# Kernel optimization log

Measured on AMD Instinct MI355X. Metric: run time of the kernel, lower is better.

The kernel has to match this reference:

```python
import jax, jax.numpy as jnp
import numpy as np

N0, N1, N2 = 30000, 90000, 60000          # nodes, edges, triangles
D_IN, D_OUT, HEADS = 256, 128, 4
NNZ0, NNZ1, NNZ2 = 960000, 180000, 180000  # sparse incidence nnz


def setup_inputs() -> dict:
    key = jax.random.key(0)
    ks = jax.random.split(key, 18)
    s = 0.05
    return {
        "x0": jax.random.normal(ks[0], (N0, D_IN), dtype=jnp.float32),
        "x1": jax.random.normal(ks[1], (N1, D_IN), dtype=jnp.float32),
        "x2": jax.random.normal(ks[2], (N2, D_IN), dtype=jnp.float32),
        "rows0": jax.random.randint(ks[3], (NNZ0,), 0, N0),
        "cols0": jax.random.randint(ks[4], (NNZ0,), 0, N0),
        "rows1": jax.random.randint(ks[5], (NNZ1,), 0, N0),
        "cols1": jax.random.randint(ks[6], (NNZ1,), 0, N1),
        "rows2": jax.random.randint(ks[7], (NNZ2,), 0, N0),
        "cols2": jax.random.randint(ks[8], (NNZ2,), 0, N2),
        # per-head parameters (SATLayer_regular), stacked on leading head axis
        "W1": jax.random.normal(ks[9], (HEADS, D_IN, D_OUT), dtype=jnp.float32) * s,
        "b1": jax.random.normal(ks[10], (HEADS, D_OUT), dtype=jnp.float32) * s,
        "a1_w": jax.random.normal(ks[11], (HEADS, D_OUT), dtype=jnp.float32) * s,
        "a1_b": jax.random.normal(ks[12], (HEADS,), dtype=jnp.float32) * s,
        "a2_w": jax.random.normal(ks[13], (HEADS, D_OUT), dtype=jnp.float32) * s,
        "a2_b": jax.random.normal(ks[14], (HEADS,), dtype=jnp.float32) * s,
        "Wagg": jax.random.normal(ks[15], (HEADS, 4 * D_OUT, D_OUT), dtype=jnp.float32) * s,
        "bagg": jax.random.normal(ks[16], (HEADS, D_OUT), dtype=jnp.float32) * s,
    }


def reference(x0, x1, x2, rows0, cols0, rows1, cols1, rows2, cols2,
              W1, b1, a1_w, a1_b, a2_w, a2_b, Wagg, bagg):
    n0 = x0.shape[0]

    def sat_head(W1h, b1h, a1wh, a1bh, a2wh, a2bh, Waggh, baggh):
        # shared Linearlayer1 + ReLU applied to all simplex levels
        xi0 = jax.nn.relu(x0 @ W1h + b1h)   # [n0, d]
        xj1 = jax.nn.relu(x1 @ W1h + b1h)   # [n1, d]
        xj2 = jax.nn.relu(x2 @ W1h + b1h)   # [n2, d]
        a1 = xi0 @ a1wh + a1bh              # [n0] attention source term

        def attention_agg(xj, rows, cols):
            a2 = xj @ a2wh + a2bh                              # [nj]
            att = jax.nn.sigmoid(a1[rows] + a2[cols])          # [nnz]
            msg = att[:, None] * xj[cols]                      # [nnz, d]
            return jax.ops.segment_sum(msg, rows, num_segments=n0)

        agg0 = attention_agg(xi0, rows0, cols0)
        agg1 = attention_agg(xj1, rows1, cols1)
        agg2 = attention_agg(xj2, rows2, cols2)
        cat = jnp.concatenate([xi0, agg0, agg1, agg2], axis=1)  # [n0, 4d]
        return cat @ Waggh + baggh                              # [n0, d]

    # stack over heads, then mean (layer0_1 + torch.mean)
    outs = jax.vmap(sat_head)(W1, b1, a1_w, a1_b, a2_w, a2_b, Wagg, bagg)
    return jnp.mean(outs, axis=0)
```

## Files before the change

### kernel.cpp

```cpp
#include <hip/hip_runtime.h>

typedef __attribute__((ext_vector_type(8))) short short8;
typedef __attribute__((ext_vector_type(4))) float f32x4;
typedef unsigned short ushort_t;
typedef unsigned int uint32;

#define N0 30000
#define N1 90000
#define N2 60000
#define P0 30208
#define S1OFF 30208
#define S2OFF 120320
#define MPAD 180352
#define MT0 236
#define MT1 704
#define MT2 469
#define MT64Y 2818
#define NE0 960000
#define NE1 180000
#define NE2 180000
#define CSTRIDE 30720

__device__ __forceinline__ float bf2f(ushort_t u) {
    union { uint32 i; float f; } v; v.i = ((uint32)u) << 16; return v.f;
}
__device__ __forceinline__ ushort_t f2bf(float f) {
    union { float f; uint32 i; } v; v.f = f;
    uint32 x = v.i;
    x += ((x >> 16) & 1u) + 0x7FFFu;
    return (ushort_t)(x >> 16);
}

__global__ __launch_bounds__(256) void prep_w(const float* __restrict__ W1,
                                              const float* __restrict__ Wagg,
                                              const float* __restrict__ bagg,
                                              ushort_t* __restrict__ W1t,
                                              ushort_t* __restrict__ Wgt,
                                              ushort_t* __restrict__ WgtC,
                                              float* __restrict__ bsum) {
    int idx = blockIdx.x * blockDim.x + threadIdx.x;
    if (idx < 131072) {
        int h = idx >> 15, rem = idx & 32767, n = rem >> 8, k = rem & 255;
        W1t[idx] = f2bf(W1[((size_t)h * 256 + k) * 128 + n]);
    }
    if (idx < 196608) {
        int h = idx / 49152, rem = idx % 49152;
        int l = rem / 16384, rem2 = rem % 16384, n = rem2 >> 7, k = rem2 & 127;
        Wgt[idx] = f2bf(Wagg[((size_t)h * 512 + (l + 1) * 128 + k) * 128 + n]);
    }
    if (idx < 65536) {
        int n = idx >> 9, kk = idx & 511, h = kk >> 7, k = kk & 127;
        WgtC[idx] = f2bf(Wagg[((size_t)h * 512 + k) * 128 + n]);
    }
    if (idx < 128) {
        float s = 0.f;
        #pragma unroll
        for (int h = 0; h < 4; ++h) s += bagg[h * 128 + idx];
        bsum[idx] = s;
    }
}

__global__ __launch_bounds__(256) void csr_zero(int* __restrict__ cur) {
    int i = blockIdx.x * blockDim.x + threadIdx.x;
    if (i < 3 * CSTRIDE) cur[i] = 0;
}

__global__ __launch_bounds__(256) void csr_hist(const int* __restrict__ rows, int nE,
                                                int* __restrict__ cur) {
    int i = blockIdx.x * blockDim.x + threadIdx.x;
    if (i < nE) atomicAdd(cur + rows[i], 1);
}

__global__ __launch_bounds__(1024) void csr_scan(int* __restrict__ curA,
                                                 int* __restrict__ rowPtrA,
                                                 int nE0, int nE1, int nE2) {
    __shared__ int ssum[1024];
    const int b = blockIdx.x;
    int* cur = curA + b * CSTRIDE;
    int* rowPtr = rowPtrA + b * CSTRIDE;
    const int nE = (b == 0) ? nE0 : (b == 1 ? nE1 : nE2);
    const int t = threadIdx.x;
    const int base = t * 30;
    int loc[30];
    int s = 0;
    #pragma unroll
    for (int i = 0; i < 30; ++i) {
        int r = base + i;
        int v = (r < N0) ? cur[r] : 0;
        loc[i] = s; s += v;
    }
    ssum[t] = s;
    __syncthreads();
    for (int off = 1; off < 1024; off <<= 1) {
        int v = (t >= off) ? ssum[t - off] : 0;
        __syncthreads();
        ssum[t] += v;
        __syncthreads();
    }
    int carry = (t == 0) ? 0 : ssum[t - 1];
    #pragma unroll
    for (int i = 0; i < 30; ++i) {
        int r = base + i;
        if (r < N0) {
            int p = carry + loc[i];
            rowPtr[r] = p;
            cur[r] = p;
        }
    }
    if (t == 0) rowPtr[N0] = nE;
}

__global__ __launch_bounds__(256) void csr_scatter(const int* __restrict__ rows,
                                                   const int* __restrict__ cols,
                                                   int nE, int Sl,
                                                   int* __restrict__ cur,
                                                   int* __restrict__ sortedCg) {
    int i = blockIdx.x * blockDim.x + threadIdx.x;
    if (i < nE) {
        int pos = atomicAdd(cur + rows[i], 1);
        sortedCg[pos] = Sl + cols[i];
    }
}

__global__ __launch_bounds__(256, 3)
void gemm_y(const float* __restrict__ x0, const float* __restrict__ x1,
            const float* __restrict__ x2,
            const ushort_t* __restrict__ W1t, const float* __restrict__ b1,
            ushort_t* __restrict__ Y)
{
    __shared__ ushort_t As[64 * 256];
    __shared__ ushort_t Bs[2][128 * 40];
    const int tid = threadIdx.x;
    const int lane = tid & 63;
    const int wn = tid >> 6;
    const int l15 = lane & 15, lg = lane >> 4;
    const int r0 = blockIdx.x * 64;

    const float* src; int jbase, nreal;
    if (r0 < P0)          { src = x0; jbase = r0;         nreal = N0; }
    else if (r0 < S2OFF)  { src = x1; jbase = r0 - S1OFF; nreal = N1; }
    else                  { src = x2; jbase = r0 - S2OFF; nreal = N2; }

    #pragma unroll
    for (int p = 0; p < 8; ++p) {
        int chunk = tid + p * 256;
        int row = chunk >> 5, c = chunk & 31;
        int j = jbase + row;
        ushort_t o[8] __attribute__((aligned(16)));
        if (j < nreal) {
            const float4 v0 = *(const float4*)(src + (size_t)j * 256 + c * 8);
            const float4 v1 = *(const float4*)(src + (size_t)j * 256 + c * 8 + 4);
            o[0] = f2bf(v0.x); o[1] = f2bf(v0.y); o[2] = f2bf(v0.z); o[3] = f2bf(v0.w);
            o[4] = f2bf(v1.x); o[5] = f2bf(v1.y); o[6] = f2bf(v1.z); o[7] = f2bf(v1.w);
        } else {
            #pragma unroll
            for (int i = 0; i < 8; ++i) o[i] = 0;
        }
        *(uint4*)(As + row * 256 + ((c ^ (row & 7)) << 3)) = *(const uint4*)o;
    }

    const int hh = wn >> 1;
    const int nbase = (wn & 1) * 64;

    #pragma unroll 1
    for (int hp = 0; hp < 2; ++hp) {
        f32x4 acc[4][4] = {};
        #pragma unroll 1
        for (int kt = 0; kt < 256; kt += 32) {
            __syncthreads();
            #pragma unroll
            for (int q = 0; q < 4; ++q) {
                int id = tid + q * 256;
                int bh = id >> 9, rem = id & 511;
                int n = rem >> 2, c = rem & 3;
                *(uint4*)(Bs[bh] + n * 40 + c * 8) =
                    *(const uint4*)(W1t + (hp * 2 + bh) * 32768 + n * 256 + kt + c * 8);
            }
            __syncthreads();

            short8 af[4], bf[4];
            #pragma unroll
            for (int m = 0; m < 4; ++m) {
                int row = m * 16 + l15;
                af[m] = *(const short8*)(As + row * 256 + ((((kt >> 3) + lg) ^ (row & 7)) << 3));
            }
            #pragma unroll
            for (int nf = 0; nf < 4; ++nf) {
                int nrow = nbase + nf * 16 + l15;
                bf[nf] = *(const short8*)(Bs[hh] + nrow * 40 + lg * 8);
            }
            #pragma unroll
            for (int m = 0; m < 4; ++m)
                #pragma unroll
                for (int nf = 0; nf < 4; ++nf)
                    acc[m][nf] = __builtin_amdgcn_mfma_f32_16x16x32_bf16(af[m], bf[nf], acc[m][nf], 0, 0, 0);
        }
        int h = hp * 2 + hh;
        #pragma unroll
        for (int nf = 0; nf < 4; ++nf) {
            int col = nbase + nf * 16 + l15;
            float bb = b1[h * 128 + col];
            #pragma unroll
            for (int m = 0; m < 4; ++m)
            #pragma unroll
            for (int j = 0; j < 4; ++j) {
                int row = r0 + m * 16 + lg * 4 + j;
                float v = acc[m][nf][j] + bb;
                v = v > 0.f ? v : 0.f;
                Y[(size_t)row * 512 + h * 128 + col] = f2bf(v);
            }
        }
    }
}

template<int EPI>
__global__ __launch_bounds__(256)
void gemm_k(const ushort_t* A, int ldA, int strideA,
            const ushort_t* __restrict__ B, int K, int strideB,
            ushort_t* outBF, int outLd, int strideOut,
            float* __restrict__ outF,
            const float* __restrict__ bias, int strideBias,
            int rowGuard)
{
    __shared__ ushort_t As[128 * 40];
    __shared__ ushort_t Bs[128 * 40];
    const int tid = threadIdx.x;
    const int lane = tid & 63;
    const int wid = tid >> 6;
    const int wm = wid >> 1, wn = wid & 1;
    const int r0 = blockIdx.x * 128;
    const int l15 = lane & 15, lg = lane >> 4;

    A += (size_t)blockIdx.y * strideA;
    B += (size_t)blockIdx.y * strideB;
    if (outBF) outBF += (size_t)blockIdx.y * strideOut;
    if (bias) bias += (size_t)blockIdx.y * strideBias;

    f32x4 acc[4][4] = {};

    for (int kt = 0; kt < K; kt += 32) {
        #pragma unroll
        for (int c = 0; c < 2; ++c) {
            int idx = tid + c * 256;
            int row = idx >> 2, kc = idx & 3;
            uint4 va = *(const uint4*)(A + (size_t)(r0 + row) * ldA + kt + kc * 8);
            *(uint4*)(As + row * 40 + kc * 8) = va;
            uint4 vb = *(const uint4*)(B + (size_t)row * K + kt + kc * 8);
            *(uint4*)(Bs + row * 40 + kc * 8) = vb;
        }
        __syncthreads();
        short8 af[4], bfr[4];
        #pragma unroll
        for (int m = 0; m < 4; ++m)
            af[m] = *(const short8*)(As + (wm * 64 + m * 16 + l15) * 40 + lg * 8);
        #pragma unroll
        for (int n = 0; n < 4; ++n)
            bfr[n] = *(const short8*)(Bs + (wn * 64 + n * 16 + l15) * 40 + lg * 8);
        #pragma unroll
        for (int m = 0; m < 4; ++m)
            #pragma unroll
            for (int n = 0; n < 4; ++n)
                acc[m][n] = __builtin_amdgcn_mfma_f32_16x16x32_bf16(af[m], bfr[n], acc[m][n], 0, 0, 0);
        __syncthreads();
    }

    #pragma unroll
    for (int m = 0; m < 4; ++m)
    #pragma unroll
    for (int n = 0; n < 4; ++n)
    #pragma unroll
    for (int j = 0; j < 4; ++j) {
        int row = r0 + wm * 64 + m * 16 + lg * 4 + j;
        int col = wn * 64 + n * 16 + l15;
        float v = acc[m][n][j];
        if (EPI == 1) {
            outBF[(size_t)row * outLd + col] = f2bf(v);
        } else {
            if (row < rowGuard) outF[(size_t)row * 128 + col] = 0.25f * (v + bias[col]);
        }
    }
}

__global__ __launch_bounds__(256)
void gemm_init(const ushort_t* __restrict__ A,
               const ushort_t* __restrict__ B,
               float* __restrict__ outF,
               const float* __restrict__ bias)
{
    __shared__ ushort_t As[128 * 40];
    __shared__ ushort_t Bs[128 * 40];
    const int tid = threadIdx.x;
    const int lane = tid & 63;
    const int wid = tid >> 6;
    const int wm = wid >> 1, wn = wid & 1;
    const int r0 = blockIdx.x * 128;
    const int l15 = lane & 15, lg = lane >> 4;

    f32x4 acc[4][4] = {};

    for (int kt = 0; kt < 512; kt += 32) {
        #pragma unroll
        for (int c = 0; c < 2; ++c) {
            int idx = tid + c * 256;
            int row = idx >> 2, kc = idx & 3;
            uint4 va = *(const uint4*)(A + (size_t)(r0 + row) * 512 + kt + kc * 8);
            *(uint4*)(As + row * 40 + kc * 8) = va;
            uint4 vb = *(const uint4*)(B + (size_t)row * 512 + kt + kc * 8);
            *(uint4*)(Bs + row * 40 + kc * 8) = vb;
        }
        __syncthreads();
        short8 af[4], bfr[4];
        #pragma unroll
        for (int m = 0; m < 4; ++m)
            af[m] = *(const short8*)(As + (wm * 64 + m * 16 + l15) * 40 + lg * 8);
        #pragma unroll
        for (int n = 0; n < 4; ++n)
            bfr[n] = *(const short8*)(Bs + (wn * 64 + n * 16 + l15) * 40 + lg * 8);
        #pragma unroll
        for (int m = 0; m < 4; ++m)
            #pragma unroll
            for (int n = 0; n < 4; ++n)
                acc[m][n] = __builtin_amdgcn_mfma_f32_16x16x32_bf16(af[m], bfr[n], acc[m][n], 0, 0, 0);
        __syncthreads();
    }

    #pragma unroll
    for (int m = 0; m < 4; ++m)
    #pragma unroll
    for (int n = 0; n < 4; ++n)
    #pragma unroll
    for (int j = 0; j < 4; ++j) {
        int row = r0 + wm * 64 + m * 16 + lg * 4 + j;
        int col = wn * 64 + n * 16 + l15;
        if (row < N0) outF[(size_t)row * 128 + col] = 0.25f * (acc[m][n][j] + bias[col]);
    }
}

__global__ __launch_bounds__(256) void attn_coef(const ushort_t* __restrict__ Y,
                                                 const float* __restrict__ a1w,
                                                 const float* __restrict__ a1b,
                                                 const float* __restrict__ a2w,
                                                 const float* __restrict__ a2b,
                                                 float* __restrict__ a1o,
                                                 float* __restrict__ a2o) {
    int tid = threadIdx.x, lane = tid & 63, wid = tid >> 6;
    int R = blockIdx.x * 4 + wid;
    int h = lane >> 4, s = lane & 15;
    uint4 v = *(const uint4*)(Y + (size_t)R * 512 + h * 128 + s * 8);
    const ushort_t* u = (const ushort_t*)&v;
    float x[8];
    #pragma unroll
    for (int i = 0; i < 8; ++i) x[i] = bf2f(u[i]);
    float d2 = 0.f;
    #pragma unroll
    for (int i = 0; i < 8; ++i) d2 += x[i] * a2w[h * 128 + s * 8 + i];
    #pragma unroll
    for (int off = 1; off < 16; off <<= 1) d2 += __shfl_xor(d2, off);
    if (s == 0) a2o[(size_t)h * MPAD + R] = d2 + a2b[h];
    if (R < N0) {
        float d1 = 0.f;
        #pragma unroll
        for (int i = 0; i < 8; ++i) d1 += x[i] * a1w[h * 128 + s * 8 + i];
        #pragma unroll
        for (int off = 1; off < 16; off <<= 1) d1 += __shfl_xor(d1, off);
        if (s == 0) a1o[(size_t)h * P0 + R] = d1 + a1b[h];
    }
}

__global__ __launch_bounds__(256) void pull_agg(const int* __restrict__ rowPtr,
                                                const int* __restrict__ sortedCg,
                                                const float* __restrict__ a1,
                                                const float* __restrict__ a2,
                                                const ushort_t* __restrict__ z,
                                                float* __restrict__ out) {
    int w = blockIdx.x * 4 + (threadIdx.x >> 6);
    if (w >= N0) return;
    const int lane = threadIdx.x & 63;
    const int h = lane >> 4, g = lane & 15;

    const float a1r = a1[(size_t)h * P0 + w];
    const float* a2h = a2 + (size_t)h * MPAD;
    int beg = rowPtr[w], end = rowPtr[w + 1];

    float acc[8] = {0.f, 0.f, 0.f, 0.f, 0.f, 0.f, 0.f, 0.f};
    int e = beg;
    for (; e + 1 < end; e += 2) {
        int cg0 = sortedCg[e], cg1 = sortedCg[e + 1];
        float s0 = a1r + a2h[cg0];
        float s1 = a1r + a2h[cg1];
        float att0 = 0.25f / (1.f + __expf(-s0));
        float att1 = 0.25f / (1.f + __expf(-s1));
        uint4 v0 = *(const uint4*)(z + (size_t)cg0 * 512 + lane * 8);
        uint4 v1 = *(const uint4*)(z + (size_t)cg1 * 512 + lane * 8);
        const ushort_t* u0 = (const ushort_t*)&v0;
        const ushort_t* u1 = (const ushort_t*)&v1;
        #pragma unroll
        for (int j = 0; j < 8; ++j)
            acc[j] += att0 * bf2f(u0[j]) + att1 * bf2f(u1[j]);
    }
    if (e < end) {
        int cg = sortedCg[e];
        float s = a1r + a2h[cg];
        float att = 0.25f / (1.f + __expf(-s));
        uint4 v = *(const uint4*)(z + (size_t)cg * 512 + lane * 8);
        const ushort_t* u = (const ushort_t*)&v;
        #pragma unroll
        for (int j = 0; j < 8; ++j) acc[j] += att * bf2f(u[j]);
    }
    #pragma unroll
    for (int j = 0; j < 8; ++j) {
        acc[j] += __shfl_xor(acc[j], 16);
        acc[j] += __shfl_xor(acc[j], 32);
    }
    float2* p = (float2*)(out + (size_t)w * 128 + g * 8 + h * 2);
    float2 o = *p;
    o.x += acc[h * 2 + 0];
    o.y += acc[h * 2 + 1];
    *p = o;
}

extern "C" void kernel_launch(void* const* d_in, const int* in_sizes, int n_in,
                              void* d_out, int out_size, void* d_ws, size_t ws_size,
                              hipStream_t stream) {
    const float* x0   = (const float*)d_in[0];
    const float* x1   = (const float*)d_in[1];
    const float* x2   = (const float*)d_in[2];
    const int* rows0  = (const int*)d_in[3];
    const int* cols0  = (const int*)d_in[4];
    const int* rows1  = (const int*)d_in[5];
    const int* cols1  = (const int*)d_in[6];
    const int* rows2  = (const int*)d_in[7];
    const int* cols2  = (const int*)d_in[8];
    const float* W1   = (const float*)d_in[9];
    const float* b1   = (const float*)d_in[10];
    const float* a1w  = (const float*)d_in[11];
    const float* a1b  = (const float*)d_in[12];
    const float* a2w  = (const float*)d_in[13];
    const float* a2b  = (const float*)d_in[14];
    const float* Wagg = (const float*)d_in[15];
    const float* bagg = (const float*)d_in[16];
    float* out = (float*)d_out;
    char* ws = (char*)d_ws;

    ushort_t* Y      = (ushort_t*)(ws);
    float*    a1o    = (float*)(ws + 184680448);
    float*    a2o    = (float*)(ws + 185163776);
    ushort_t* W1t    = (ushort_t*)(ws + 188049408);
    ushort_t* Wgt    = (ushort_t*)(ws + 188311552);
    ushort_t* WgtC   = (ushort_t*)(ws + 188704768);
    float*    bsum   = (float*)(ws + 188835840);
    int*      cur    = (int*)(ws + 188836352);
    int*      rowPtr = (int*)(ws + 189204992);
    int*      srtCg  = (int*)(ws + 189573632);

    int* cur0 = cur,    * cur1 = cur + CSTRIDE,    * cur2 = cur + 2 * CSTRIDE;
    int* rp0  = rowPtr, * rp1  = rowPtr + CSTRIDE, * rp2  = rowPtr + 2 * CSTRIDE;
    int* srt0 = srtCg,  * srt1 = srtCg + NE0,      * srt2 = srtCg + NE0 + NE1;

    csr_zero<<<(3 * CSTRIDE + 255) / 256, 256, 0, stream>>>(cur);
    csr_hist<<<(NE0 + 255) / 256, 256, 0, stream>>>(rows0, NE0, cur0);
    csr_hist<<<(NE1 + 255) / 256, 256, 0, stream>>>(rows1, NE1, cur1);
    csr_hist<<<(NE2 + 255) / 256, 256, 0, stream>>>(rows2, NE2, cur2);
    csr_scan<<<3, 1024, 0, stream>>>(cur, rowPtr, NE0, NE1, NE2);
    csr_scatter<<<(NE0 + 255) / 256, 256, 0, stream>>>(rows0, cols0, NE0, 0,     cur0, srt0);
    csr_scatter<<<(NE1 + 255) / 256, 256, 0, stream>>>(rows1, cols1, NE1, S1OFF, cur1, srt1);
    csr_scatter<<<(NE2 + 255) / 256, 256, 0, stream>>>(rows2, cols2, NE2, S2OFF, cur2, srt2);

    prep_w<<<768, 256, 0, stream>>>(W1, Wagg, bagg, W1t, Wgt, WgtC, bsum);
    gemm_y<<<MT64Y, 256, 0, stream>>>(x0, x1, x2, W1t, b1, Y);

    attn_coef<<<MPAD / 4, 256, 0, stream>>>(Y, a1w, a1b, a2w, a2b, a1o, a2o);
    gemm_init<<<MT0, 256, 0, stream>>>(Y, WgtC, out, bsum);

    gemm_k<1><<<dim3(MT0, 4), 256, 0, stream>>>(
        Y, 512, 128, Wgt + 0 * 16384, 128, 3 * 16384, Y, 512, 128, nullptr, nullptr, 0, 0);
    gemm_k<1><<<dim3(MT1, 4), 256, 0, stream>>>(
        Y + (size_t)S1OFF * 512, 512, 128, Wgt + 1 * 16384, 128, 3 * 16384,
        Y + (size_t)S1OFF * 512, 512, 128, nullptr, nullptr, 0, 0);
    gemm_k<1><<<dim3(MT2, 4), 256, 0, stream>>>(
        Y + (size_t)S2OFF * 512, 512, 128, Wgt + 2 * 16384, 128, 3 * 16384,
        Y + (size_t)S2OFF * 512, 512, 128, nullptr, nullptr, 0, 0);

    pull_agg<<<(N0 + 3) / 4, 256, 0, stream>>>(rp0, srt0, a1o, a2o, Y, out);
    pull_agg<<<(N0 + 3) / 4, 256, 0, stream>>>(rp1, srt1, a1o, a2o, Y, out);
    pull_agg<<<(N0 + 3) / 4, 256, 0, stream>>>(rp2, srt2, a1o, a2o, Y, out);
}
```

Measured before the change: 659.0 us.

## Fuse attention coefficients into gemm_y epilogue, merge per-level GEMMs, prefetch B

Computes the a1/a2 attention dot products inside the gemm_y epilogue using shuffle reductions and atomics, removing the separate attn_coef pass that re-read Y. A new coef_init kernel seeds those outputs with the biases. The three per-level projection GEMMs become a single gemm_z launch that picks its weight slice from the row-tile index. gemm_y also prefetches the next B tile into registers, and pull_agg is unrolled to four edges per iteration. In exchange it adds many atomics and extra register pressure in gemm_y.

After: 801.0 us. +21.5%, slower.

```diff
diff --git a/kernel.cpp b/kernel.cpp
--- a/kernel.cpp
+++ b/kernel.cpp
@@ -13,8 +13,7 @@
 #define S2OFF 120320
 #define MPAD 180352
 #define MT0 236
-#define MT1 704
-#define MT2 469
+#define MT_ALL 1409
 #define MT64Y 2818
 #define NE0 960000
 #define NE1 180000
@@ -58,6 +57,15 @@
         for (int h = 0; h < 4; ++h) s += bagg[h * 128 + idx];
         bsum[idx] = s;
     }
+}
+
+__global__ __launch_bounds__(256) void coef_init(const float* __restrict__ a1b,
+                                                 const float* __restrict__ a2b,
+                                                 float* __restrict__ a1o,
+                                                 float* __restrict__ a2o) {
+    int i = blockIdx.x * blockDim.x + threadIdx.x;
+    if (i < 4 * MPAD) a2o[i] = a2b[i / MPAD];
+    if (i < 4 * P0)   a1o[i] = a1b[i / P0];
 }
 
 __global__ __launch_bounds__(256) void csr_zero(int* __restrict__ cur) {
@@ -126,6 +134,8 @@
 void gemm_y(const float* __restrict__ x0, const float* __restrict__ x1,
             const float* __restrict__ x2,
             const ushort_t* __restrict__ W1t, const float* __restrict__ b1,
+            const float* __restrict__ a1w, const float* __restrict__ a2w,
+            float* __restrict__ a1o, float* __restrict__ a2o,
             ushort_t* __restrict__ Y)
 {
     __shared__ ushort_t As[64 * 256];
@@ -135,9 +145,10 @@
     const int wn = tid >> 6;
     const int l15 = lane & 15, lg = lane >> 4;
     const int r0 = blockIdx.x * 64;
+    const bool isL0 = (r0 < P0);
 
     const float* src; int jbase, nreal;
-    if (r0 < P0)          { src = x0; jbase = r0;         nreal = N0; }
+    if (isL0)             { src = x0; jbase = r0;         nreal = N0; }
     else if (r0 < S2OFF)  { src = x1; jbase = r0 - S1OFF; nreal = N1; }
     else                  { src = x2; jbase = r0 - S2OFF; nreal = N2; }
 
@@ -162,6 +173,18 @@
     const int hh = wn >> 1;
     const int nbase = (wn & 1) * 64;
 
+    uint4 breg[4];
+    auto loadB = [&](int hp_, int kt_) {
+        #pragma unroll
+        for (int q = 0; q < 4; ++q) {
+            int id = tid + q * 256;
+            int bh = id >> 9, rem = id & 511;
+            int n = rem >> 2, cc = rem & 3;
+            breg[q] = *(const uint4*)(W1t + (hp_ * 2 + bh) * 32768 + n * 256 + kt_ + cc * 8);
+        }
+    };
+    loadB(0, 0);
+
     #pragma unroll 1
     for (int hp = 0; hp < 2; ++hp) {
         f32x4 acc[4][4] = {};
@@ -172,11 +195,12 @@
             for (int q = 0; q < 4; ++q) {
                 int id = tid + q * 256;
                 int bh = id >> 9, rem = id & 511;
-                int n = rem >> 2, c = rem & 3;
-                *(uint4*)(Bs[bh] + n * 40 + c * 8) =
-                    *(const uint4*)(W1t + (hp * 2 + bh) * 32768 + n * 256 + kt + c * 8);
+                int n = rem >> 2, cc = rem & 3;
+                *(uint4*)(Bs[bh] + n * 40 + cc * 8) = breg[q];
             }
             __syncthreads();
+            if (kt < 224)       loadB(hp, kt + 32);
+            else if (hp == 0)   loadB(1, 0);
 
             short8 af[4], bf[4];
             #pragma unroll
@@ -196,10 +220,15 @@
                     acc[m][nf] = __builtin_amdgcn_mfma_f32_16x16x32_bf16(af[m], bf[nf], acc[m][nf], 0, 0, 0);
         }
         int h = hp * 2 + hh;
+        float d1p[16], d2p[16];
+        #pragma unroll
+        for (int i = 0; i < 16; ++i) { d1p[i] = 0.f; d2p[i] = 0.f; }
         #pragma unroll
         for (int nf = 0; nf < 4; ++nf) {
             int col = nbase + nf * 16 + l15;
             float bb = b1[h * 128 + col];
+            float w1c = a1w[h * 128 + col];
+            float w2c = a2w[h * 128 + col];
             #pragma unroll
             for (int m = 0; m < 4; ++m)
             #pragma unroll
@@ -208,19 +237,33 @@
                 float v = acc[m][nf][j] + bb;
                 v = v > 0.f ? v : 0.f;
                 Y[(size_t)row * 512 + h * 128 + col] = f2bf(v);
-            }
-        }
-    }
-}
-
-template<int EPI>
+                d1p[m * 4 + j] += v * w1c;
+                d2p[m * 4 + j] += v * w2c;
+            }
+        }
+        #pragma unroll
+        for (int i = 0; i < 16; ++i) {
+            #pragma unroll
+            for (int off = 1; off < 16; off <<= 1) {
+                d1p[i] += __shfl_xor(d1p[i], off);
+                d2p[i] += __shfl_xor(d2p[i], off);
+            }
+        }
+        if (l15 == 0) {
+            #pragma unroll
+            for (int m = 0; m < 4; ++m)
+            #pragma unroll
+            for (int j = 0; j < 4; ++j) {
+                int row = r0 + m * 16 + lg * 4 + j;
+                atomicAdd(a2o + (size_t)h * MPAD + row, d2p[m * 4 + j]);
+                if (isL0) atomicAdd(a1o + (size_t)h * P0 + row, d1p[m * 4 + j]);
+            }
+        }
+    }
+}
+
 __global__ __launch_bounds__(256)
-void gemm_k(const ushort_t* A, int ldA, int strideA,
-            const ushort_t* __restrict__ B, int K, int strideB,
-            ushort_t* outBF, int outLd, int strideOut,
-            float* __restrict__ outF,
-            const float* __restrict__ bias, int strideBias,
-            int rowGuard)
+void gemm_z(ushort_t* Y, const ushort_t* __restrict__ Wgt)
 {
     __shared__ ushort_t As[128 * 40];
     __shared__ ushort_t Bs[128 * 40];
@@ -229,23 +272,22 @@
     const int wid = tid >> 6;
     const int wm = wid >> 1, wn = wid & 1;
     const int r0 = blockIdx.x * 128;
+    const int h = blockIdx.y;
     const int l15 = lane & 15, lg = lane >> 4;
-
-    A += (size_t)blockIdx.y * strideA;
-    B += (size_t)blockIdx.y * strideB;
-    if (outBF) outBF += (size_t)blockIdx.y * strideOut;
-    if (bias) bias += (size_t)blockIdx.y * strideBias;
+    const int l = (r0 < P0) ? 0 : (r0 < S2OFF ? 1 : 2);
+    const ushort_t* B = Wgt + ((h * 3 + l) << 14);
+    ushort_t* A = Y + (size_t)h * 128;
 
     f32x4 acc[4][4] = {};
 
-    for (int kt = 0; kt < K; kt += 32) {
+    for (int kt = 0; kt < 128; kt += 32) {
         #pragma unroll
         for (int c = 0; c < 2; ++c) {
             int idx = tid + c * 256;
             int row = idx >> 2, kc = idx & 3;
-            uint4 va = *(const uint4*)(A + (size_t)(r0 + row) * ldA + kt + kc * 8);
+            uint4 va = *(const uint4*)(A + (size_t)(r0 + row) * 512 + kt + kc * 8);
             *(uint4*)(As + row * 40 + kc * 8) = va;
-            uint4 vb = *(const uint4*)(B + (size_t)row * K + kt + kc * 8);
+            uint4 vb = *(const uint4*)(B + (size_t)row * 128 + kt + kc * 8);
             *(uint4*)(Bs + row * 40 + kc * 8) = vb;
         }
         __syncthreads();
@@ -272,12 +314,7 @@
     for (int j = 0; j < 4; ++j) {
         int row = r0 + wm * 64 + m * 16 + lg * 4 + j;
         int col = wn * 64 + n * 16 + l15;
-        float v = acc[m][n][j];
-        if (EPI == 1) {
-            outBF[(size_t)row * outLd + col] = f2bf(v);
-        } else {
-            if (row < rowGuard) outF[(size_t)row * 128 + col] = 0.25f * (v + bias[col]);
-        }
+        A[(size_t)row * 512 + col] = f2bf(acc[m][n][j]);
     }
 }
 
@@ -336,37 +373,6 @@
     }
 }
 
-__global__ __launch_bounds__(256) void attn_coef(const ushort_t* __restrict__ Y,
-                                                 const float* __restrict__ a1w,
-                                                 const float* __restrict__ a1b,
-                                                 const float* __restrict__ a2w,
-                                                 const float* __restrict__ a2b,
-                                                 float* __restrict__ a1o,
-                                                 float* __restrict__ a2o) {
-    int tid = threadIdx.x, lane = tid & 63, wid = tid >> 6;
-    int R = blockIdx.x * 4 + wid;
-    int h = lane >> 4, s = lane & 15;
-    uint4 v = *(const uint4*)(Y + (size_t)R * 512 + h * 128 + s * 8);
-    const ushort_t* u = (const ushort_t*)&v;
-    float x[8];
-    #pragma unroll
-    for (int i = 0; i < 8; ++i) x[i] = bf2f(u[i]);
-    float d2 = 0.f;
-    #pragma unroll
-    for (int i = 0; i < 8; ++i) d2 += x[i] * a2w[h * 128 + s * 8 + i];
-    #pragma unroll
-    for (int off = 1; off < 16; off <<= 1) d2 += __shfl_xor(d2, off);
-    if (s == 0) a2o[(size_t)h * MPAD + R] = d2 + a2b[h];
-    if (R < N0) {
-        float d1 = 0.f;
-        #pragma unroll
-        for (int i = 0; i < 8; ++i) d1 += x[i] * a1w[h * 128 + s * 8 + i];
-        #pragma unroll
-        for (int off = 1; off < 16; off <<= 1) d1 += __shfl_xor(d1, off);
-        if (s == 0) a1o[(size_t)h * P0 + R] = d1 + a1b[h];
-    }
-}
-
 __global__ __launch_bounds__(256) void pull_agg(const int* __restrict__ rowPtr,
                                                 const int* __restrict__ sortedCg,
                                                 const float* __restrict__ a1,
@@ -384,24 +390,30 @@
 
     float acc[8] = {0.f, 0.f, 0.f, 0.f, 0.f, 0.f, 0.f, 0.f};
     int e = beg;
-    for (; e + 1 < end; e += 2) {
-        int cg0 = sortedCg[e], cg1 = sortedCg[e + 1];
-        float s0 = a1r + a2h[cg0];
-        float s1 = a1r + a2h[cg1];
-        float att0 = 0.25f / (1.f + __expf(-s0));
-        float att1 = 0.25f / (1.f + __expf(-s1));
+    int n4 = beg + ((end - beg) & ~3);
+    for (; e < n4; e += 4) {
+        int cg0 = sortedCg[e],     cg1 = sortedCg[e + 1];
+        int cg2 = sortedCg[e + 2], cg3 = sortedCg[e + 3];
+        float att0 = 0.25f / (1.f + __expf(-(a1r + a2h[cg0])));
+        float att1 = 0.25f / (1.f + __expf(-(a1r + a2h[cg1])));
+        float att2 = 0.25f / (1.f + __expf(-(a1r + a2h[cg2])));
+        float att3 = 0.25f / (1.f + __expf(-(a1r + a2h[cg3])));
         uint4 v0 = *(const uint4*)(z + (size_t)cg0 * 512 + lane * 8);
         uint4 v1 = *(const uint4*)(z + (size_t)cg1 * 512 + lane * 8);
+        uint4 v2 = *(const uint4*)(z + (size_t)cg2 * 512 + lane * 8);
+        uint4 v3 = *(const uint4*)(z + (size_t)cg3 * 512 + lane * 8);
         const ushort_t* u0 = (const ushort_t*)&v0;
         const ushort_t* u1 = (const ushort_t*)&v1;
+        const ushort_t* u2 = (const ushort_t*)&v2;
+        const ushort_t* u3 = (const ushort_t*)&v3;
         #pragma unroll
         for (int j = 0; j < 8; ++j)
-            acc[j] += att0 * bf2f(u0[j]) + att1 * bf2f(u1[j]);
-    }
-    if (e < end) {
+            acc[j] += att0 * bf2f(u0[j]) + att1 * bf2f(u1[j])
+                    + att2 * bf2f(u2[j]) + att3 * bf2f(u3[j]);
+    }
+    for (; e < end; ++e) {
         int cg = sortedCg[e];
-        float s = a1r + a2h[cg];
-        float att = 0.25f / (1.f + __expf(-s));
+        float att = 0.25f / (1.f + __expf(-(a1r + a2h[cg])));
         uint4 v = *(const uint4*)(z + (size_t)cg * 512 + lane * 8);
         const ushort_t* u = (const ushort_t*)&v;
         #pragma unroll
@@ -458,6 +470,7 @@
     int* srt0 = srtCg,  * srt1 = srtCg + NE0,      * srt2 = srtCg + NE0 + NE1;
 
     csr_zero<<<(3 * CSTRIDE + 255) / 256, 256, 0, stream>>>(cur);
+    coef_init<<<(4 * MPAD + 255) / 256, 256, 0, stream>>>(a1b, a2b, a1o, a2o);
     csr_hist<<<(NE0 + 255) / 256, 256, 0, stream>>>(rows0, NE0, cur0);
     csr_hist<<<(NE1 + 255) / 256, 256, 0, stream>>>(rows1, NE1, cur1);
     csr_hist<<<(NE2 + 255) / 256, 256, 0, stream>>>(rows2, NE2, cur2);
@@ -467,19 +480,11 @@
     csr_scatter<<<(NE2 + 255) / 256, 256, 0, stream>>>(rows2, cols2, NE2, S2OFF, cur2, srt2);
 
     prep_w<<<768, 256, 0, stream>>>(W1, Wagg, bagg, W1t, Wgt, WgtC, bsum);
-    gemm_y<<<MT64Y, 256, 0, stream>>>(x0, x1, x2, W1t, b1, Y);
-
-    attn_coef<<<MPAD / 4, 256, 0, stream>>>(Y, a1w, a1b, a2w, a2b, a1o, a2o);
+    gemm_y<<<MT64Y, 256, 0, stream>>>(x0, x1, x2, W1t, b1, a1w, a2w, a1o, a2o, Y);
+
     gemm_init<<<MT0, 256, 0, stream>>>(Y, WgtC, out, bsum);
 
-    gemm_k<1><<<dim3(MT0, 4), 256, 0, stream>>>(
-        Y, 512, 128, Wgt + 0 * 16384, 128, 3 * 16384, Y, 512, 128, nullptr, nullptr, 0, 0);
-    gemm_k<1><<<dim3(MT1, 4), 256, 0, stream>>>(
-        Y + (size_t)S1OFF * 512, 512, 128, Wgt + 1 * 16384, 128, 3 * 16384,
-        Y + (size_t)S1OFF * 512, 512, 128, nullptr, nullptr, 0, 0);
-    gemm_k<1><<<dim3(MT2, 4), 256, 0, stream>>>(
-        Y + (size_t)S2OFF * 512, 512, 128, Wgt + 2 * 16384, 128, 3 * 16384,
-        Y + (size_t)S2OFF * 512, 512, 128, nullptr, nullptr, 0, 0);
+    gemm_z<<<dim3(MT_ALL, 4), 256, 0, stream>>>(Y, Wgt);
 
     pull_agg<<<(N0 + 3) / 4, 256, 0, stream>>>(rp0, srt0, a1o, a2o, Y, out);
     pull_agg<<<(N0 + 3) / 4, 256, 0, stream>>>(rp1, srt1, a1o, a2o, Y, out);
```
